# Kernel optimization log

Hardware: AMD Instinct MI355X
Metric: run time of the kernel (lower is better)

The kernel has to match this reference:

```python
import jax, jax.numpy as jnp
import numpy as np

N_NODES = 100000
N_EDGES = 800000
H_DIM = 128
E_DIM = 32
N_LAYER = 3


def setup_inputs() -> dict:
    key = jax.random.key(0)
    ks = jax.random.split(key, 5)
    x = jax.random.normal(ks[0], (N_NODES, H_DIM), dtype=jnp.float32)
    edge_index = jax.random.randint(ks[1], (2, N_EDGES), 0, N_NODES, dtype=jnp.int64)
    edge_attr = jax.random.normal(ks[2], (N_EDGES, E_DIM), dtype=jnp.float32)
    fan_in = 2 * H_DIM + E_DIM
    # torch Linear weight layout: [out_features, in_features]
    Wm = jax.random.normal(ks[3], (N_LAYER, H_DIM, fan_in), dtype=jnp.float32) / jnp.sqrt(fan_in)
    bm = jax.random.normal(ks[4], (N_LAYER, H_DIM), dtype=jnp.float32) * 0.01
    return {"x": x, "edge_index": edge_index, "edge_attr": edge_attr, "Wm": Wm, "bm": bm}


def reference(x, edge_index, edge_attr, Wm, bm):
    # PyG flow='source_to_target': row 0 = source (j), row 1 = target (i)
    src = edge_index[0]
    dst = edge_index[1]
    n_nodes = x.shape[0]
    n_layer = Wm.shape[0]
    for l in range(n_layer):  # small fixed layer count
        # message: m_ij = Linear(cat[x_j, x_i, edge_attr])
        m = jnp.concatenate([x[src], x[dst], edge_attr], axis=1)  # [E, 2h+e]
        m = jnp.einsum('ef,hf->eh', m, Wm[l]) + bm[l]             # [E, h]
        # aggr='add': scatter-add messages to target nodes
        x = jax.ops.segment_sum(m, dst, num_segments=n_nodes)     # [N, h]
        x = jax.nn.leaky_relu(x, negative_slope=0.01)
    # residual_connection='none' -> no-op; activate_last=True
    x = jax.nn.leaky_relu(x, negative_slope=0.01)
    return x
```

## Files before the change

kernel.cpp:

```cpp
#include <hip/hip_runtime.h>

#define N_NODES 100000
#define NP      100096
#define N_EDGES 800000
#define HD 128
#define ED 32
#define FAN 288
#define NL 3

#define SCHUNK 2048
#define SBLK   ((N_NODES + SCHUNK - 1) / SCHUNK)

typedef short bf16x8 __attribute__((ext_vector_type(8)));
typedef short bf16x4 __attribute__((ext_vector_type(4)));
typedef float f32x4  __attribute__((ext_vector_type(4)));

__device__ inline float b2f(short s) {
    unsigned u = ((unsigned)(unsigned short)s) << 16;
    return __builtin_bit_cast(float, u);
}
__device__ inline short f2b(float f) {
    unsigned u = __builtin_bit_cast(unsigned, f);
    unsigned r = u + 0x7FFFu + ((u >> 16) & 1u);
    return (short)(r >> 16);
}


__global__ void count_kernel(const int* __restrict__ dst, int* __restrict__ deg) {
    int e = blockIdx.x * 256 + threadIdx.x;
    if (e < N_EDGES) atomicAdd(&deg[dst[e]], 1);
}

__global__ void scan_reduce(const int* __restrict__ deg, int* __restrict__ bsum) {
    __shared__ int ws[4];
    const int tid = threadIdx.x;
    int i0 = blockIdx.x * SCHUNK + tid * 8;
    int t = 0;
    #pragma unroll
    for (int j = 0; j < 8; ++j) {
        int i = i0 + j;
        if (i < N_NODES) t += deg[i];
    }
    #pragma unroll
    for (int off = 32; off >= 1; off >>= 1) t += __shfl_down(t, off, 64);
    if ((tid & 63) == 0) ws[tid >> 6] = t;
    __syncthreads();
    if (tid == 0) bsum[blockIdx.x] = ws[0] + ws[1] + ws[2] + ws[3];
}

__global__ void scan_mid(const int* __restrict__ bsum, int* __restrict__ boff,
                         int* __restrict__ ptr) {
    int lane = threadIdx.x;
    int v = (lane < SBLK) ? bsum[lane] : 0;
    int s = v;
    #pragma unroll
    for (int off = 1; off < 64; off <<= 1) {
        int t = __shfl_up(s, off, 64);
        if (lane >= off) s += t;
    }
    if (lane < SBLK) boff[lane] = s - v;
    if (lane == 63) ptr[N_NODES] = s;
}

__global__ void scan_final(const int* __restrict__ deg, const int* __restrict__ boff,
                           int* __restrict__ ptr, int* __restrict__ cursor) {
    __shared__ int wsum[4];
    const int tid = threadIdx.x;
    const int lane = tid & 63, wid = tid >> 6;
    int i0 = blockIdx.x * SCHUNK + tid * 8;
    int v[8]; int tsum = 0;
    #pragma unroll
    for (int j = 0; j < 8; ++j) {
        int i = i0 + j;
        v[j] = (i < N_NODES) ? deg[i] : 0;
        tsum += v[j];
    }
    int s = tsum;
    #pragma unroll
    for (int off = 1; off < 64; off <<= 1) {
        int t = __shfl_up(s, off, 64);
        if (lane >= off) s += t;
    }
    if (lane == 63) wsum[wid] = s;
    __syncthreads();
    int woff = 0;
    #pragma unroll
    for (int w = 0; w < 4; ++w) if (w < wid) woff += wsum[w];
    int excl = boff[blockIdx.x] + woff + (s - tsum);
    #pragma unroll
    for (int j = 0; j < 8; ++j) {
        int i = i0 + j;
        if (i < N_NODES) { ptr[i] = excl; cursor[i] = excl; }
        excl += v[j];
    }
}

__global__ void fill_kernel(const int* __restrict__ src, const int* __restrict__ dst,
                            int* __restrict__ cursor, int2* __restrict__ csr2) {
    int e = blockIdx.x * 256 + threadIdx.x;
    if (e < N_EDGES) {
        int d = dst[e];
        int slot = atomicAdd(&cursor[d], 1);
        csr2[slot] = make_int2(src[e], e);
    }
}

__global__ void permute_eattr(const int2* __restrict__ csr2, const float* __restrict__ eattr,
                              short* __restrict__ ecsr) {
    int idx = blockIdx.x * 256 + threadIdx.x;
    int s = idx >> 3;
    int g = idx & 7;
    if (s >= N_EDGES) return;
    int e = csr2[s].y;
    float4 v = *reinterpret_cast<const float4*>(eattr + (size_t)e * ED + g * 4);
    bf16x4 o;
    o[0] = f2b(v.x); o[1] = f2b(v.y); o[2] = f2b(v.z); o[3] = f2b(v.w);
    *reinterpret_cast<bf16x4*>(ecsr + (size_t)s * ED + g * 4) = o;
}

__global__ void edge_sum(const short* __restrict__ ecsr, const int* __restrict__ ptr,
                         short* __restrict__ agge, float* __restrict__ degf) {
    int node = blockIdx.x * 32 + (threadIdx.x >> 3);
    int g = threadIdx.x & 7;
    if (node >= N_NODES) return;
    int s0 = ptr[node], s1 = ptr[node + 1];
    float a[4] = {};
    for (int s = s0; s < s1; ++s) {
        bf16x4 v = *reinterpret_cast<const bf16x4*>(ecsr + (size_t)s * ED + g * 4);
        #pragma unroll
        for (int j = 0; j < 4; ++j) a[j] += b2f(v[j]);
    }
    bf16x4 o;
    #pragma unroll
    for (int j = 0; j < 4; ++j) o[j] = f2b(a[j]);
    *reinterpret_cast<bf16x4*>(agge + (size_t)node * ED + g * 4) = o;
    if (g == 0) degf[node] = (float)(s1 - s0);
}

__global__ void wconv_kernel(const float* __restrict__ Wm, short* __restrict__ Wb) {
    int idx = blockIdx.x * 256 + threadIdx.x;
    if (idx < NL * HD * FAN) Wb[idx] = f2b(Wm[idx]);
}

__global__ void xconv_kernel(const float* __restrict__ x, const float* __restrict__ degf,
                             short* __restrict__ xb, short* __restrict__ xd) {
    int i4 = blockIdx.x * 256 + threadIdx.x;
    if (i4 >= N_NODES * (HD / 4)) return;
    int row = i4 >> 5;
    float d = degf[row];
    float4 v = reinterpret_cast<const float4*>(x)[i4];
    bf16x4 o, od;
    float vv[4] = {v.x, v.y, v.z, v.w};
    #pragma unroll
    for (int j = 0; j < 4; ++j) {
        short s = f2b(vv[j]);
        o[j] = s;
        od[j] = f2b(b2f(s) * d);
    }
    *reinterpret_cast<bf16x4*>(xb + (size_t)i4 * 4) = o;
    *reinterpret_cast<bf16x4*>(xd + (size_t)i4 * 4) = od;
}

#define TM 64

__global__ __launch_bounds__(256) void fused_layer(
    const int* __restrict__ ptr, const int2* __restrict__ csr2,
    const short* __restrict__ xprev,
    const short* __restrict__ xdeg,
    const short* __restrict__ agge,
    const float* __restrict__ degf,
    const short* __restrict__ Wb,
    const float* __restrict__ b,
    float* __restrict__ out_f32,
    short* __restrict__ out_x,
    short* __restrict__ out_xd,
    int last)
{
    __shared__ char As[TM * 256];
    const int tid = threadIdx.x;
    const int m0 = blockIdx.x * TM;

    {
        const int ng = tid >> 4, g = tid & 15;
        #pragma unroll
        for (int i = 0; i < 4; ++i) {
            int row = i * 16 + ng;
            int node = m0 + row;
            float acc0[8] = {}, acc1[8] = {};
            if (node < N_NODES) {
                int s0 = ptr[node], s1 = ptr[node + 1];
                int s = s0;
                int i0 = (s < s1) ? csr2[s].x : 0;
                int i1 = (s + 1 < s1) ? csr2[s + 1].x : 0;
                for (; s + 2 <= s1;) {
                    bf16x8 v0 = *reinterpret_cast<const bf16x8*>(xprev + (size_t)i0 * HD + g * 8);
                    bf16x8 v1 = *reinterpret_cast<const bf16x8*>(xprev + (size_t)i1 * HD + g * 8);
                    s += 2;
                    i0 = (s < s1) ? csr2[s].x : 0;
                    i1 = (s + 1 < s1) ? csr2[s + 1].x : 0;
                    #pragma unroll
                    for (int j = 0; j < 8; ++j) acc0[j] += b2f(v0[j]);
                    #pragma unroll
                    for (int j = 0; j < 8; ++j) acc1[j] += b2f(v1[j]);
                }
                if (s < s1) {
                    bf16x8 v0 = *reinterpret_cast<const bf16x8*>(xprev + (size_t)i0 * HD + g * 8);
                    #pragma unroll
                    for (int j = 0; j < 8; ++j) acc0[j] += b2f(v0[j]);
                }
            }
            bf16x8 o;
            #pragma unroll
            for (int j = 0; j < 8; ++j) o[j] = f2b(acc0[j] + acc1[j]);
            int byte = row * 256 + g * 16;
            byte ^= (row & 7) << 4;
            *reinterpret_cast<bf16x8*>(As + byte) = o;
        }
    }
    __syncthreads();

    const int w = tid >> 6, lane = tid & 63;
    const int wy = w >> 1, wx = w & 1;
    const int l15 = lane & 15, lq = lane >> 4;
    const int kb = lq * 8;

    f32x4 acc[2][4];
    #pragma unroll
    for (int i = 0; i < 2; ++i)
        #pragma unroll
        for (int j = 0; j < 4; ++j) acc[i][j] = (f32x4){0.f, 0.f, 0.f, 0.f};

    #pragma unroll
    for (int kt = 0; kt < 4; ++kt) {
        bf16x8 a[2], bf[4];
        #pragma unroll
        for (int mf = 0; mf < 2; ++mf) {
            int row = wy * 32 + mf * 16 + l15;
            int byte = row * 256 + kt * 64 + kb * 2;
            byte ^= (row & 7) << 4;
            a[mf] = *reinterpret_cast<const bf16x8*>(As + byte);
        }
        #pragma unroll
        for (int nf = 0; nf < 4; ++nf) {
            int c = wx * 64 + nf * 16 + l15;
            bf[nf] = *reinterpret_cast<const bf16x8*>(Wb + (size_t)c * FAN + kt * 32 + kb);
        }
        #pragma unroll
        for (int mf = 0; mf < 2; ++mf)
            #pragma unroll
            for (int nf = 0; nf < 4; ++nf)
                acc[mf][nf] = __builtin_amdgcn_mfma_f32_16x16x32_bf16(
                    a[mf], bf[nf], acc[mf][nf], 0, 0, 0);
    }
    #pragma unroll
    for (int kt = 4; kt < 9; ++kt) {
        bf16x8 a[2], bf[4];
        #pragma unroll
        for (int mf = 0; mf < 2; ++mf) {
            size_t arow = (size_t)(m0 + wy * 32 + mf * 16 + l15);
            a[mf] = (kt < 8)
                ? *reinterpret_cast<const bf16x8*>(xdeg + arow * HD + (kt * 32 - 128) + kb)
                : *reinterpret_cast<const bf16x8*>(agge + arow * ED + kb);
        }
        #pragma unroll
        for (int nf = 0; nf < 4; ++nf) {
            int c = wx * 64 + nf * 16 + l15;
            bf[nf] = *reinterpret_cast<const bf16x8*>(Wb + (size_t)c * FAN + kt * 32 + kb);
        }
        #pragma unroll
        for (int mf = 0; mf < 2; ++mf)
            #pragma unroll
            for (int nf = 0; nf < 4; ++nf)
                acc[mf][nf] = __builtin_amdgcn_mfma_f32_16x16x32_bf16(
                    a[mf], bf[nf], acc[mf][nf], 0, 0, 0);
    }

    #pragma unroll
    for (int mf = 0; mf < 2; ++mf) {
        int r0 = m0 + wy * 32 + mf * 16 + lq * 4;
        float dg[4];
        #pragma unroll
        for (int j = 0; j < 4; ++j)
            dg[j] = (r0 + j < N_NODES) ? degf[r0 + j] : 0.f;
        #pragma unroll
        for (int nf = 0; nf < 4; ++nf) {
            int c = wx * 64 + nf * 16 + l15;
            float bc = b[c];
            #pragma unroll
            for (int j = 0; j < 4; ++j) {
                int row = r0 + j;
                if (row >= N_NODES) continue;
                float v = acc[mf][nf][j] + dg[j] * bc;
                v = (v >= 0.f) ? v : 0.01f * v;
                if (last) {
                    v = (v >= 0.f) ? v : 0.01f * v;
                    out_f32[(size_t)row * HD + c] = v;
                } else {
                    short xb = f2b(v);
                    out_x[(size_t)row * HD + c] = xb;
                    out_xd[(size_t)row * HD + c] = f2b(b2f(xb) * dg[j]);
                }
            }
        }
    }
}

extern "C" void kernel_launch(void* const* d_in, const int* in_sizes, int n_in,
                              void* d_out, int out_size, void* d_ws, size_t ws_size,
                              hipStream_t stream) {
    const float* x_in  = (const float*)d_in[0];
    const int*   ei    = (const int*)d_in[1];
    const float* eattr = (const float*)d_in[2];
    const float* Wm    = (const float*)d_in[3];
    const float* bm    = (const float*)d_in[4];
    float* out = (float*)d_out;

    char* ws = (char*)d_ws;
    size_t off = 0;
    auto alloc = [&](size_t bytes) -> void* {
        void* p = ws + off;
        off = (off + bytes + 255) & ~(size_t)255;
        return p;
    };
    short* x0     = (short*)alloc((size_t)NP * HD * 2);
    short* x1     = (short*)alloc((size_t)NP * HD * 2);
    short* xdeg   = (short*)alloc((size_t)NP * HD * 2);
    short* agge   = (short*)alloc((size_t)NP * ED * 2);
    float* degf   = (float*)alloc((size_t)NP * 4);
    int*   deg    = (int*)alloc((size_t)N_NODES * 4);
    int*   ptr    = (int*)alloc((size_t)(N_NODES + 1) * 4);
    int*   cursor = (int*)alloc((size_t)N_NODES * 4);
    int2*  csr2   = (int2*)alloc((size_t)N_EDGES * 8);
    short* Wb     = (short*)alloc((size_t)NL * HD * FAN * 2);
    int*   bsum   = (int*)alloc((size_t)SBLK * 4);
    int*   boff   = (int*)alloc((size_t)SBLK * 4);

    short* ecsr = x0;

    const int* src = ei;
    const int* dst = ei + N_EDGES;

    hipMemsetAsync(deg, 0, (size_t)N_NODES * 4, stream);
    count_kernel<<<(N_EDGES + 255) / 256, 256, 0, stream>>>(dst, deg);
    scan_reduce<<<SBLK, 256, 0, stream>>>(deg, bsum);
    scan_mid<<<1, 64, 0, stream>>>(bsum, boff, ptr);
    scan_final<<<SBLK, 256, 0, stream>>>(deg, boff, ptr, cursor);
    fill_kernel<<<(N_EDGES + 255) / 256, 256, 0, stream>>>(src, dst, cursor, csr2);
    permute_eattr<<<(N_EDGES * 8 + 255) / 256, 256, 0, stream>>>(csr2, eattr, ecsr);
    edge_sum<<<(N_NODES + 31) / 32, 256, 0, stream>>>(ecsr, ptr, agge, degf);
    wconv_kernel<<<(NL * HD * FAN + 255) / 256, 256, 0, stream>>>(Wm, Wb);
    xconv_kernel<<<(N_NODES * (HD / 4) + 255) / 256, 256, 0, stream>>>(x_in, degf, x0, xdeg);

    short* xping[2] = {x0, x1};
    for (int l = 0; l < NL; ++l) {
        fused_layer<<<NP / TM, 256, 0, stream>>>(
            ptr, csr2, xping[l & 1], xdeg, agge, degf,
            Wb + (size_t)l * HD * FAN, bm + (size_t)l * HD,
            out, xping[(l + 1) & 1], xdeg, (l == NL - 1) ? 1 : 0);
    }
}
```

Before: 372.9 us.

## Fuse edge-attr permute into edge_sum, unroll gathers by four, halve layer tile

```diff
diff --git a/kernel.cpp b/kernel.cpp
--- a/kernel.cpp
+++ b/kernel.cpp
@@ -105,34 +105,50 @@
     }
 }
 
-__global__ void permute_eattr(const int2* __restrict__ csr2, const float* __restrict__ eattr,
-                              short* __restrict__ ecsr) {
-    int idx = blockIdx.x * 256 + threadIdx.x;
-    int s = idx >> 3;
-    int g = idx & 7;
-    if (s >= N_EDGES) return;
-    int e = csr2[s].y;
-    float4 v = *reinterpret_cast<const float4*>(eattr + (size_t)e * ED + g * 4);
-    bf16x4 o;
-    o[0] = f2b(v.x); o[1] = f2b(v.y); o[2] = f2b(v.z); o[3] = f2b(v.w);
-    *reinterpret_cast<bf16x4*>(ecsr + (size_t)s * ED + g * 4) = o;
-}
-
-__global__ void edge_sum(const short* __restrict__ ecsr, const int* __restrict__ ptr,
+__global__ void edge_sum(const int2* __restrict__ csr2, const int* __restrict__ ptr,
+                         const float* __restrict__ eattr,
                          short* __restrict__ agge, float* __restrict__ degf) {
     int node = blockIdx.x * 32 + (threadIdx.x >> 3);
     int g = threadIdx.x & 7;
     if (node >= N_NODES) return;
     int s0 = ptr[node], s1 = ptr[node + 1];
-    float a[4] = {};
-    for (int s = s0; s < s1; ++s) {
-        bf16x4 v = *reinterpret_cast<const bf16x4*>(ecsr + (size_t)s * ED + g * 4);
-        #pragma unroll
-        for (int j = 0; j < 4; ++j) a[j] += b2f(v[j]);
+    float4 a0 = make_float4(0.f,0.f,0.f,0.f), a1 = make_float4(0.f,0.f,0.f,0.f);
+    int s = s0;
+    int e0 = (s     < s1) ? csr2[s].y     : 0;
+    int e1 = (s + 1 < s1) ? csr2[s + 1].y : 0;
+    int e2 = (s + 2 < s1) ? csr2[s + 2].y : 0;
+    int e3 = (s + 3 < s1) ? csr2[s + 3].y : 0;
+    while (s + 4 <= s1) {
+        float4 v0 = *reinterpret_cast<const float4*>(eattr + (size_t)e0 * ED + g * 4);
+        float4 v1 = *reinterpret_cast<const float4*>(eattr + (size_t)e1 * ED + g * 4);
+        float4 v2 = *reinterpret_cast<const float4*>(eattr + (size_t)e2 * ED + g * 4);
+        float4 v3 = *reinterpret_cast<const float4*>(eattr + (size_t)e3 * ED + g * 4);
+        s += 4;
+        e0 = (s     < s1) ? csr2[s].y     : 0;
+        e1 = (s + 1 < s1) ? csr2[s + 1].y : 0;
+        e2 = (s + 2 < s1) ? csr2[s + 2].y : 0;
+        e3 = (s + 3 < s1) ? csr2[s + 3].y : 0;
+        a0.x += v0.x; a0.y += v0.y; a0.z += v0.z; a0.w += v0.w;
+        a1.x += v1.x; a1.y += v1.y; a1.z += v1.z; a1.w += v1.w;
+        a0.x += v2.x; a0.y += v2.y; a0.z += v2.z; a0.w += v2.w;
+        a1.x += v3.x; a1.y += v3.y; a1.z += v3.z; a1.w += v3.w;
+    }
+    int rem = s1 - s;
+    if (rem > 0) {
+        float4 v = *reinterpret_cast<const float4*>(eattr + (size_t)e0 * ED + g * 4);
+        a0.x += v.x; a0.y += v.y; a0.z += v.z; a0.w += v.w;
+    }
+    if (rem > 1) {
+        float4 v = *reinterpret_cast<const float4*>(eattr + (size_t)e1 * ED + g * 4);
+        a1.x += v.x; a1.y += v.y; a1.z += v.z; a1.w += v.w;
+    }
+    if (rem > 2) {
+        float4 v = *reinterpret_cast<const float4*>(eattr + (size_t)e2 * ED + g * 4);
+        a0.x += v.x; a0.y += v.y; a0.z += v.z; a0.w += v.w;
     }
     bf16x4 o;
-    #pragma unroll
-    for (int j = 0; j < 4; ++j) o[j] = f2b(a[j]);
+    o[0] = f2b(a0.x + a1.x); o[1] = f2b(a0.y + a1.y);
+    o[2] = f2b(a0.z + a1.z); o[3] = f2b(a0.w + a1.w);
     *reinterpret_cast<bf16x4*>(agge + (size_t)node * ED + g * 4) = o;
     if (g == 0) degf[node] = (float)(s1 - s0);
 }
@@ -161,7 +177,7 @@
     *reinterpret_cast<bf16x4*>(xd + (size_t)i4 * 4) = od;
 }
 
-#define TM 64
+#define TM 32
 
 __global__ __launch_bounds__(256) void fused_layer(
     const int* __restrict__ ptr, const int2* __restrict__ csr2,
@@ -183,30 +199,51 @@
     {
         const int ng = tid >> 4, g = tid & 15;
         #pragma unroll
-        for (int i = 0; i < 4; ++i) {
+        for (int i = 0; i < 2; ++i) {
             int row = i * 16 + ng;
             int node = m0 + row;
             float acc0[8] = {}, acc1[8] = {};
             if (node < N_NODES) {
                 int s0 = ptr[node], s1 = ptr[node + 1];
                 int s = s0;
-                int i0 = (s < s1) ? csr2[s].x : 0;
+                int i0 = (s     < s1) ? csr2[s].x     : 0;
                 int i1 = (s + 1 < s1) ? csr2[s + 1].x : 0;
-                for (; s + 2 <= s1;) {
+                int i2 = (s + 2 < s1) ? csr2[s + 2].x : 0;
+                int i3 = (s + 3 < s1) ? csr2[s + 3].x : 0;
+                while (s + 4 <= s1) {
                     bf16x8 v0 = *reinterpret_cast<const bf16x8*>(xprev + (size_t)i0 * HD + g * 8);
                     bf16x8 v1 = *reinterpret_cast<const bf16x8*>(xprev + (size_t)i1 * HD + g * 8);
-                    s += 2;
-                    i0 = (s < s1) ? csr2[s].x : 0;
+                    bf16x8 v2 = *reinterpret_cast<const bf16x8*>(xprev + (size_t)i2 * HD + g * 8);
+                    bf16x8 v3 = *reinterpret_cast<const bf16x8*>(xprev + (size_t)i3 * HD + g * 8);
+                    s += 4;
+                    i0 = (s     < s1) ? csr2[s].x     : 0;
                     i1 = (s + 1 < s1) ? csr2[s + 1].x : 0;
+                    i2 = (s + 2 < s1) ? csr2[s + 2].x : 0;
+                    i3 = (s + 3 < s1) ? csr2[s + 3].x : 0;
                     #pragma unroll
                     for (int j = 0; j < 8; ++j) acc0[j] += b2f(v0[j]);
                     #pragma unroll
                     for (int j = 0; j < 8; ++j) acc1[j] += b2f(v1[j]);
-                }
-                if (s < s1) {
-                    bf16x8 v0 = *reinterpret_cast<const bf16x8*>(xprev + (size_t)i0 * HD + g * 8);
-                    #pragma unroll
-                    for (int j = 0; j < 8; ++j) acc0[j] += b2f(v0[j]);
+                    #pragma unroll
+                    for (int j = 0; j < 8; ++j) acc0[j] += b2f(v2[j]);
+                    #pragma unroll
+                    for (int j = 0; j < 8; ++j) acc1[j] += b2f(v3[j]);
+                }
+                int rem = s1 - s;
+                if (rem > 0) {
+                    bf16x8 v = *reinterpret_cast<const bf16x8*>(xprev + (size_t)i0 * HD + g * 8);
+                    #pragma unroll
+                    for (int j = 0; j < 8; ++j) acc0[j] += b2f(v[j]);
+                }
+                if (rem > 1) {
+                    bf16x8 v = *reinterpret_cast<const bf16x8*>(xprev + (size_t)i1 * HD + g * 8);
+                    #pragma unroll
+                    for (int j = 0; j < 8; ++j) acc1[j] += b2f(v[j]);
+                }
+                if (rem > 2) {
+                    bf16x8 v = *reinterpret_cast<const bf16x8*>(xprev + (size_t)i2 * HD + g * 8);
+                    #pragma unroll
+                    for (int j = 0; j < 8; ++j) acc0[j] += b2f(v[j]);
                 }
             }
             bf16x8 o;
@@ -220,71 +257,70 @@
     __syncthreads();
 
     const int w = tid >> 6, lane = tid & 63;
-    const int wy = w >> 1, wx = w & 1;
     const int l15 = lane & 15, lq = lane >> 4;
     const int kb = lq * 8;
 
-    f32x4 acc[2][4];
+    f32x4 acc[2][2];
     #pragma unroll
     for (int i = 0; i < 2; ++i)
         #pragma unroll
-        for (int j = 0; j < 4; ++j) acc[i][j] = (f32x4){0.f, 0.f, 0.f, 0.f};
+        for (int j = 0; j < 2; ++j) acc[i][j] = (f32x4){0.f, 0.f, 0.f, 0.f};
 
     #pragma unroll
     for (int kt = 0; kt < 4; ++kt) {
-        bf16x8 a[2], bf[4];
+        bf16x8 a[2], bf[2];
         #pragma unroll
         for (int mf = 0; mf < 2; ++mf) {
-            int row = wy * 32 + mf * 16 + l15;
+            int row = mf * 16 + l15;
             int byte = row * 256 + kt * 64 + kb * 2;
             byte ^= (row & 7) << 4;
             a[mf] = *reinterpret_cast<const bf16x8*>(As + byte);
         }
         #pragma unroll
-        for (int nf = 0; nf < 4; ++nf) {
-            int c = wx * 64 + nf * 16 + l15;
+        for (int nf = 0; nf < 2; ++nf) {
+            int c = w * 32 + nf * 16 + l15;
             bf[nf] = *reinterpret_cast<const bf16x8*>(Wb + (size_t)c * FAN + kt * 32 + kb);
         }
         #pragma unroll
         for (int mf = 0; mf < 2; ++mf)
             #pragma unroll
-            for (int nf = 0; nf < 4; ++nf)
+            for (int nf = 0; nf < 2; ++nf)
                 acc[mf][nf] = __builtin_amdgcn_mfma_f32_16x16x32_bf16(
                     a[mf], bf[nf], acc[mf][nf], 0, 0, 0);
     }
     #pragma unroll
     for (int kt = 4; kt < 9; ++kt) {
-        bf16x8 a[2], bf[4];
+        bf16x8 a[2], bf[2];
         #pragma unroll
         for (int mf = 0; mf < 2; ++mf) {
-            size_t arow = (size_t)(m0 + wy * 32 + mf * 16 + l15);
+            size_t arow = (size_t)(m0 + mf * 16 + l15);
             a[mf] = (kt < 8)
                 ? *reinterpret_cast<const bf16x8*>(xdeg + arow * HD + (kt * 32 - 128) + kb)
                 : *reinterpret_cast<const bf16x8*>(agge + arow * ED + kb);
         }
         #pragma unroll
-        for (int nf = 0; nf < 4; ++nf) {
-            int c = wx * 64 + nf * 16 + l15;
+        for (int nf = 0; nf < 2; ++nf) {
+            int c = w * 32 + nf * 16 + l15;
             bf[nf] = *reinterpret_cast<const bf16x8*>(Wb + (size_t)c * FAN + kt * 32 + kb);
         }
         #pragma unroll
         for (int mf = 0; mf < 2; ++mf)
             #pragma unroll
-            for (int nf = 0; nf < 4; ++nf)
+            for (int nf = 0; nf < 2; ++nf)
                 acc[mf][nf] = __builtin_amdgcn_mfma_f32_16x16x32_bf16(
                     a[mf], bf[nf], acc[mf][nf], 0, 0, 0);
     }
 
     #pragma unroll
     for (int mf = 0; mf < 2; ++mf) {
-        int r0 = m0 + wy * 32 + mf * 16 + lq * 4;
+        int r0 = m0 + mf * 16 + lq * 4;
         float dg[4];
         #pragma unroll
         for (int j = 0; j < 4; ++j)
             dg[j] = (r0 + j < N_NODES) ? degf[r0 + j] : 0.f;
         #pragma unroll
-        for (int nf = 0; nf < 4; ++nf) {
-            int c = wx * 64 + nf * 16 + l15;
+        for (int nf = 0; nf < 2; ++nf) {
+            int c = w * 32 + nf * 16 + l15;
             float bc = b[c];
             #pragma unroll
             for (int j = 0; j < 4; ++j) {
@@ -335,8 +371,6 @@
     int*   bsum   = (int*)alloc((size_t)SBLK * 4);
     int*   boff   = (int*)alloc((size_t)SBLK * 4);
 
-    short* ecsr = x0;
-
     const int* src = ei;
     const int* dst = ei + N_EDGES;
 
@@ -346,8 +380,7 @@
     scan_mid<<<1, 64, 0, stream>>>(bsum, boff, ptr);
     scan_final<<<SBLK, 256, 0, stream>>>(deg, boff, ptr, cursor);
     fill_kernel<<<(N_EDGES + 255) / 256, 256, 0, stream>>>(src, dst, cursor, csr2);
-    permute_eattr<<<(N_EDGES * 8 + 255) / 256, 256, 0, stream>>>(csr2, eattr, ecsr);
-    edge_sum<<<(N_NODES + 31) / 32, 256, 0, stream>>>(ecsr, ptr, agge, degf);
+    edge_sum<<<(N_NODES + 31) / 32, 256, 0, stream>>>(csr2, ptr, eattr, agge, degf);
     wconv_kernel<<<(NL * HD * FAN + 255) / 256, 256, 0, stream>>>(Wm, Wb);
     xconv_kernel<<<(N_NODES * (HD / 4) + 255) / 256, 256, 0, stream>>>(x_in, degf, x0, xdeg);
 
```

Result: faster. 344.1 us (-7.7%).
